# Kernel tuning notes

Hardware: AMD Instinct MI355X
Metric: run time of the kernel (lower is better)

## Reference

```python
import jax, jax.numpy as jnp
import numpy as np

B, T, D, H = 8, 2048, 1024, 1024

def setup_inputs() -> dict:
    key = jax.random.key(0)
    k1, k2, k3, k4 = jax.random.split(key, 4)
    scale = 1.0 / np.sqrt(D)
    return {
        "x": jax.random.normal(k1, (B, T, D), dtype=jnp.float32),
        "Wq": jax.random.normal(k2, (D, H), dtype=jnp.float32) * scale,
        "Wk": jax.random.normal(k3, (D, H), dtype=jnp.float32) * scale,
        "Wv": jax.random.normal(k4, (D, H), dtype=jnp.float32) * scale,
    }

def reference(x, Wq, Wk, Wv):
    # Single-head causal self-attention (dropout in eval mode = identity)
    q = jnp.einsum('btd,dh->bth', x, Wq)
    k = jnp.einsum('btd,dh->bth', x, Wk)
    v = jnp.einsum('btd,dh->bth', x, Wv)
    inv_sqrt_h = 1.0 / jnp.sqrt(jnp.asarray(q.shape[-1], q.dtype))
    scores = jnp.einsum('bqh,bkh->bqk', q, k) * inv_sqrt_h  # [B, T, T]
    Tq = scores.shape[-1]
    causal = jnp.tril(jnp.ones((Tq, Tq), dtype=bool))
    scores = jnp.where(causal, scores, jnp.asarray(-jnp.inf, scores.dtype))
    weights = jax.nn.softmax(scores, axis=-1)
    return jnp.einsum('bqk,bkh->bqh', weights, v)
```

## Files before the change

### kernel.cpp

```cpp
#include <hip/hip_runtime.h>

#define Bn 8
#define Tn 2048
#define Dn 1024
#define Hn 1024
#define Mn (Bn * Tn)

typedef __attribute__((ext_vector_type(8))) short bf16x8;
typedef __attribute__((ext_vector_type(4))) short short4v;
typedef __attribute__((ext_vector_type(16))) float f32x16;
typedef __attribute__((ext_vector_type(4))) float f32x4;

__device__ __forceinline__ unsigned short f2bf(float f) {
  union { float f; unsigned int u; } v; v.f = f;
  unsigned int u = v.u;
  u += 0x7FFFu + ((u >> 16) & 1u);
  return (unsigned short)(u >> 16);
}
__device__ __forceinline__ float bf2f(unsigned short h) {
  union { unsigned int u; float f; } v; v.u = ((unsigned int)h) << 16;
  return v.f;
}

__device__ __forceinline__ void gload_lds16(const unsigned short* g, unsigned short* l) {
  __builtin_amdgcn_global_load_lds((const __attribute__((address_space(1))) void*)g,
                                   (__attribute__((address_space(3))) void*)l, 16, 0, 0);
}


__device__ __forceinline__ void stage128x32s(const unsigned short* gbase, size_t row_stride,
                                             unsigned short* lds, int wave, int lane) {
#pragma unroll
  for (int c = 0; c < 2; ++c) {
    int rl = c * 16 + (lane >> 2);
    int pos = (lane & 3) ^ (rl & 3) ^ ((rl >> 2) & 3);
    const unsigned short* g = gbase + (size_t)(wave * 32 + rl) * row_stride + pos * 8;
    gload_lds16(g, lds + (wave * 32 + c * 16) * 32);
  }
}
__device__ __forceinline__ void stage128x64s(const unsigned short* gbase, size_t row_stride,
                                             unsigned short* lds0, unsigned short* lds1,
                                             int wave, int lane) {
  stage128x32s(gbase, row_stride, lds0, wave, lane);
  stage128x32s(gbase + 32, row_stride, lds1, wave, lane);
}

__device__ __forceinline__ void stage256x32s(const unsigned short* gbase, size_t row_stride,
                                             unsigned short* lds, int wave, int lane) {
#pragma unroll
  for (int c = 0; c < 2; ++c) {
    int rl = c * 16 + (lane >> 2);
    int pos = (lane & 3) ^ (rl & 3) ^ ((rl >> 2) & 3);
    const unsigned short* g = gbase + (size_t)(wave * 32 + rl) * row_stride + pos * 8;
    gload_lds16(g, lds + (wave * 32 + c * 16) * 32);
  }
}

__device__ __forceinline__ void mma_bk32(const unsigned short* lA, const unsigned short* lB,
                                         int wr, int wc, int l32, int half,
                                         f32x16 acc[2][2]) {
#pragma unroll
  for (int kk = 0; kk < 2; ++kk) {
    const int pos = (kk * 2 + half) ^ (l32 & 3) ^ ((l32 >> 2) & 3);
    bf16x8 af[2], bfr[2];
#pragma unroll
    for (int m = 0; m < 2; ++m)
      af[m] = *(const bf16x8*)&lA[(wr + m * 32 + l32) * 32 + pos * 8];
#pragma unroll
    for (int n = 0; n < 2; ++n)
      bfr[n] = *(const bf16x8*)&lB[(wc + n * 32 + l32) * 32 + pos * 8];
#pragma unroll
    for (int m = 0; m < 2; ++m)
#pragma unroll
      for (int n = 0; n < 2; ++n)
        acc[m][n] = __builtin_amdgcn_mfma_f32_32x32x16_bf16(af[m], bfr[n], acc[m][n], 0, 0, 0);
  }
}

__global__ __launch_bounds__(256) void k_convert(const float* __restrict__ in,
                                                 unsigned short* __restrict__ out, int n4) {
  int idx = blockIdx.x * 256 + threadIdx.x;
  if (idx >= n4) return;
  float4 v = ((const float4*)in)[idx];
  short4v o;
  o.x = (short)f2bf(v.x); o.y = (short)f2bf(v.y);
  o.z = (short)f2bf(v.z); o.w = (short)f2bf(v.w);
  *(short4v*)(out + (size_t)idx * 4) = o;
}

__global__ __launch_bounds__(256) void k_cvt_w_t(const float* __restrict__ W0,
                                                 const float* __restrict__ W1,
                                                 const float* __restrict__ W2,
                                                 unsigned short* __restrict__ Wt3) {
  const int n0 = blockIdx.x * 64, k0 = blockIdx.y * 64, w = blockIdx.z;
  const float* W = (w == 0) ? W0 : (w == 1) ? W1 : W2;
  unsigned short* Wt = Wt3 + (size_t)w * Hn * Dn;
  __shared__ unsigned short lT[64 * 65];
  const int tid = threadIdx.x;
#pragma unroll
  for (int p = 0; p < 2; ++p) {
    int o = tid + p * 256;
    int r = o >> 3, c = (o & 7) * 8;
    const float* src = W + (size_t)(k0 + r) * Hn + n0 + c;
    float4 v0 = *(const float4*)src;
    float4 v1 = *(const float4*)(src + 4);
    unsigned short* d = &lT[r * 65 + c];
    d[0] = f2bf(v0.x); d[1] = f2bf(v0.y); d[2] = f2bf(v0.z); d[3] = f2bf(v0.w);
    d[4] = f2bf(v1.x); d[5] = f2bf(v1.y); d[6] = f2bf(v1.z); d[7] = f2bf(v1.w);
  }
  __syncthreads();
#pragma unroll
  for (int p = 0; p < 2; ++p) {
    int o = tid + p * 256;
    int r2 = o >> 3, c2 = (o & 7) * 8;
    bf16x8 v;
#pragma unroll
    for (int s = 0; s < 8; ++s) v[s] = (short)lT[(c2 + s) * 65 + r2];
    *(bf16x8*)(Wt + (size_t)(n0 + r2) * Dn + k0 + c2) = v;
  }
}

__global__ __launch_bounds__(512, 2) void gemm_qkv(const unsigned short* __restrict__ A,
                                                   const unsigned short* __restrict__ Wt3,
                                                   unsigned short* __restrict__ Q,
                                                   unsigned short* __restrict__ Kb,
                                                   unsigned short* __restrict__ Vt) {
  const int f = blockIdx.x;
  const int c = f & 7;
  const int q = f >> 3;
  const int nn = q % 12;
  const int w = nn >> 2;
  const int n0 = (nn & 3) * 256;
  const int m0 = ((q / 12) * 8 + c) * 256;
  const unsigned short* Bw = Wt3 + (size_t)w * Hn * Dn;
  __shared__ unsigned short lds[2][4][256 * 32];
  const int tid = threadIdx.x;
  const int lane = tid & 63, wave = tid >> 6;
  const int wr = (wave >> 2) * 128;
  const int wc = (wave & 3) * 64;
  const int rl15 = lane & 15, l4 = lane >> 4;
  const int csw = (l4 ^ (lane & 3) ^ ((lane >> 2) & 3)) & 3;

  f32x4 acc[8][4];
#pragma unroll
  for (int m = 0; m < 8; ++m)
#pragma unroll
    for (int n = 0; n < 4; ++n) acc[m][n] = (f32x4)(0.f);

  const unsigned short* Ab = A + (size_t)m0 * Dn;
  const unsigned short* Bb = Bw + (size_t)n0 * Dn;

  auto stage_tile = [&](int kt, int d) {
#pragma unroll
    for (int h = 0; h < 2; ++h) {
      stage256x32s(Ab + kt * 64 + h * 32, Dn, &lds[d][h][0], wave, lane);
      stage256x32s(Bb + kt * 64 + h * 32, Dn, &lds[d][2 + h][0], wave, lane);
    }
  };

  auto compute_tile = [&](int d) {
    const unsigned short* pa = &lds[d][0][0];
    const unsigned short* pb = &lds[d][2][0];
    bf16x8 af[4][2], bf[4][2];
#pragma unroll
    for (int m = 0; m < 4; ++m)
#pragma unroll
      for (int h = 0; h < 2; ++h)
        af[m][h] = *(const bf16x8*)&pa[h * 8192 + (wr + m * 16 + rl15) * 32 + csw * 8];
#pragma unroll
    for (int n = 0; n < 2; ++n)
#pragma unroll
      for (int h = 0; h < 2; ++h)
        bf[n][h] = *(const bf16x8*)&pb[h * 8192 + (wc + n * 16 + rl15) * 32 + csw * 8];
    __builtin_amdgcn_s_setprio(1);
#pragma unroll
    for (int m = 0; m < 4; ++m)
#pragma unroll
      for (int n = 0; n < 2; ++n)
#pragma unroll
        for (int h = 0; h < 2; ++h)
          acc[m][n] = __builtin_amdgcn_mfma_f32_16x16x32_bf16(af[m][h], bf[n][h], acc[m][n], 0, 0, 0);
    __builtin_amdgcn_s_setprio(0);
#pragma unroll
    for (int n = 2; n < 4; ++n)
#pragma unroll
      for (int h = 0; h < 2; ++h)
        bf[n][h] = *(const bf16x8*)&pb[h * 8192 + (wc + n * 16 + rl15) * 32 + csw * 8];
    __builtin_amdgcn_s_setprio(1);
#pragma unroll
    for (int m = 0; m < 4; ++m)
#pragma unroll
      for (int n = 2; n < 4; ++n)
#pragma unroll
        for (int h = 0; h < 2; ++h)
          acc[m][n] = __builtin_amdgcn_mfma_f32_16x16x32_bf16(af[m][h], bf[n][h], acc[m][n], 0, 0, 0);
    __builtin_amdgcn_s_setprio(0);
#pragma unroll
    for (int m = 0; m < 4; ++m)
#pragma unroll
      for (int h = 0; h < 2; ++h)
        af[m][h] = *(const bf16x8*)&pa[h * 8192 + (wr + (m + 4) * 16 + rl15) * 32 + csw * 8];
    __builtin_amdgcn_s_setprio(1);
#pragma unroll
    for (int m = 0; m < 4; ++m)
#pragma unroll
      for (int n = 2; n < 4; ++n)
#pragma unroll
        for (int h = 0; h < 2; ++h)
          acc[m + 4][n] = __builtin_amdgcn_mfma_f32_16x16x32_bf16(af[m][h], bf[n][h], acc[m + 4][n], 0, 0, 0);
    __builtin_amdgcn_s_setprio(0);
    __builtin_amdgcn_s_setprio(1);
#pragma unroll
    for (int m = 0; m < 4; ++m)
#pragma unroll
      for (int n = 0; n < 2; ++n)
#pragma unroll
        for (int h = 0; h < 2; ++h)
          acc[m + 4][n] = __builtin_amdgcn_mfma_f32_16x16x32_bf16(af[m][h], bf[n][h], acc[m + 4][n], 0, 0, 0);
    __builtin_amdgcn_s_setprio(0);
  };

  stage_tile(0, 0);
  for (int kt = 0; kt < Dn / 64 - 1; ++kt) {
    const int d = kt & 1;
    __builtin_amdgcn_s_barrier();
    stage_tile(kt + 1, d ^ 1);
    asm volatile("s_waitcnt vmcnt(8)" ::: "memory");
    __builtin_amdgcn_s_barrier();
    compute_tile(d);
  }
  asm volatile("s_waitcnt vmcnt(0)" ::: "memory");
  __builtin_amdgcn_s_barrier();
  compute_tile(1);

  if (w != 2) {
    unsigned short* Cp = (w == 0) ? Q : Kb;
#pragma unroll
    for (int m = 0; m < 8; ++m) {
      const int row = m0 + wr + m * 16 + l4 * 4;
#pragma unroll
      for (int n = 0; n < 4; ++n) {
        const int col = n0 + wc + n * 16 + rl15;
#pragma unroll
        for (int r = 0; r < 4; ++r)
          Cp[(size_t)(row + r) * Hn + col] = f2bf(acc[m][n][r]);
      }
    }
  } else {
    const int bb = m0 >> 11;
    const int tb = m0 & 2047;
#pragma unroll
    for (int m = 0; m < 8; ++m) {
      const int t0 = tb + wr + m * 16 + l4 * 4;
#pragma unroll
      for (int n = 0; n < 4; ++n) {
        const int h = n0 + wc + n * 16 + rl15;
        short4v o;
        o.x = (short)f2bf(acc[m][n][0]);
        o.y = (short)f2bf(acc[m][n][1]);
        o.z = (short)f2bf(acc[m][n][2]);
        o.w = (short)f2bf(acc[m][n][3]);
        *(short4v*)(Vt + ((size_t)bb * Hn + h) * Tn + t0) = o;
      }
    }
  }
}

__global__ __launch_bounds__(256) void gemm_scores(const unsigned short* __restrict__ Q,
                                                   const unsigned short* __restrict__ K,
                                                   unsigned short* __restrict__ S) {
  const int f = blockIdx.x;
  const int b = f & 7;
  const int q = f >> 3;
  const int rt = 15 - (q & 15);
  const int ct = q >> 4;
  if (ct > rt) return;
  const int j0 = ct * 128, i0 = rt * 128;
  const unsigned short* Qb = Q + (size_t)b * Tn * Hn;
  const unsigned short* Kp = K + (size_t)b * Tn * Hn;
  unsigned short* Sb = S + (size_t)b * Tn * Tn;
  __shared__ unsigned short lA[2][128 * 32];
  __shared__ unsigned short lB[2][128 * 32];
  const int tid = threadIdx.x;
  const int lane = tid & 63, wave = tid >> 6;
  const int wr = (wave >> 1) * 64, wc = (wave & 1) * 64;
  const int l32 = lane & 31, half = lane >> 5;

  f32x16 acc[2][2];
#pragma unroll
  for (int m = 0; m < 2; ++m)
#pragma unroll
    for (int n = 0; n < 2; ++n) acc[m][n] = (f32x16)(0.f);

  for (int kt = 0; kt < Hn / 64; ++kt) {
    stage128x64s(Qb + (size_t)i0 * Hn + kt * 64, Hn, lA[0], lA[1], wave, lane);
    stage128x64s(Kp + (size_t)j0 * Hn + kt * 64, Hn, lB[0], lB[1], wave, lane);
    __syncthreads();
    mma_bk32(lA[0], lB[0], wr, wc, l32, half, acc);
    mma_bk32(lA[1], lB[1], wr, wc, l32, half, acc);
    __syncthreads();
  }
#pragma unroll
  for (int m = 0; m < 2; ++m)
#pragma unroll
    for (int n = 0; n < 2; ++n) {
      int col = j0 + wc + n * 32 + l32;
#pragma unroll
      for (int qd = 0; qd < 4; ++qd) {
        int rb = i0 + wr + m * 32 + 8 * qd + 4 * half;
#pragma unroll
        for (int rr = 0; rr < 4; ++rr) {
          int row = rb + rr;
          float e = (col <= row) ? __expf(acc[m][n][qd * 4 + rr] * 0.03125f) : 0.f;
          Sb[(size_t)row * Tn + col] = f2bf(e);
        }
      }
    }
}

__global__ __launch_bounds__(256) void k_rowsum(const unsigned short* __restrict__ S,
                                                float* __restrict__ l) {
  const int b = blockIdx.y;
  const int i = blockIdx.x * 4 + (threadIdx.x >> 6);
  const int lane = threadIdx.x & 63;
  const unsigned short* row = S + ((size_t)b * Tn + i) * (size_t)Tn;
  const int npad = ((i >> 7) + 1) << 7;
  float s = 0.f;
  for (int j0 = 0; j0 < npad; j0 += 512) {
    int j = j0 + lane * 8;
    if (j < npad) {
      bf16x8 v = *(const bf16x8*)(row + j);
#pragma unroll
      for (int t = 0; t < 8; ++t) s += bf2f((unsigned short)v[t]);
    }
  }
#pragma unroll
  for (int off = 32; off > 0; off >>= 1) s += __shfl_down(s, off);
  if (lane == 0) l[(size_t)b * Tn + i] = s;
}

__global__ __launch_bounds__(256) void gemm_out(const unsigned short* __restrict__ P,
                                                const unsigned short* __restrict__ Vt,
                                                const float* __restrict__ lbuf,
                                                float* __restrict__ O) {
  const int f = blockIdx.x;
  const int b = f & 7;
  const int q = f >> 3;
  const int n0 = (q & 7) * 128;
  const int rt = 15 - (q >> 3);
  const int i0 = rt * 128;
  const int nkt = (rt + 1) * 2;
  const unsigned short* Pb = P + (size_t)b * Tn * Tn;
  const unsigned short* Vb = Vt + (size_t)b * Tn * Hn;
  __shared__ unsigned short lA[2][128 * 32];
  __shared__ unsigned short lB[2][128 * 32];
  const int tid = threadIdx.x;
  const int lane = tid & 63, wave = tid >> 6;
  const int wr = (wave >> 1) * 64, wc = (wave & 1) * 64;
  const int l32 = lane & 31, half = lane >> 5;

  f32x16 acc[2][2];
#pragma unroll
  for (int m = 0; m < 2; ++m)
#pragma unroll
    for (int n = 0; n < 2; ++n) acc[m][n] = (f32x16)(0.f);

  for (int kt = 0; kt < nkt; ++kt) {
    stage128x64s(Pb + (size_t)i0 * Tn + kt * 64, Tn, lA[0], lA[1], wave, lane);
    stage128x64s(Vb + (size_t)n0 * Tn + kt * 64, Tn, lB[0], lB[1], wave, lane);
    __syncthreads();
    mma_bk32(lA[0], lB[0], wr, wc, l32, half, acc);
    mma_bk32(lA[1], lB[1], wr, wc, l32, half, acc);
    __syncthreads();
  }
#pragma unroll
  for (int m = 0; m < 2; ++m)
#pragma unroll
    for (int n = 0; n < 2; ++n) {
      int col = n0 + wc + n * 32 + l32;
#pragma unroll
      for (int qd = 0; qd < 4; ++qd) {
        int rb = i0 + wr + m * 32 + 8 * qd + 4 * half;
        float4 lv = *(const float4*)&lbuf[(size_t)b * Tn + rb];
#pragma unroll
        for (int rr = 0; rr < 4; ++rr) {
          float inv = 1.f / ((&lv.x)[rr]);
          O[((size_t)b * Tn + rb + rr) * Hn + col] = acc[m][n][qd * 4 + rr] * inv;
        }
      }
    }
}

extern "C" void kernel_launch(void* const* d_in, const int* in_sizes, int n_in,
                              void* d_out, int out_size, void* d_ws, size_t ws_size,
                              hipStream_t stream) {
  const float* x  = (const float*)d_in[0];
  const float* Wq = (const float*)d_in[1];
  const float* Wk = (const float*)d_in[2];
  const float* Wv = (const float*)d_in[3];
  float* out = (float*)d_out;

  char* ws = (char*)d_ws;
  const size_t MiB = 1024 * 1024;
  unsigned short* Wt3 = (unsigned short*)(ws + 0 * MiB);
  unsigned short* xb  = (unsigned short*)(ws + 6 * MiB);
  unsigned short* Qb  = (unsigned short*)(ws + 38 * MiB);
  unsigned short* Kb  = (unsigned short*)(ws + 70 * MiB);
  unsigned short* Vt  = (unsigned short*)(ws + 102 * MiB);
  unsigned short* S   = (unsigned short*)(ws + 134 * MiB);
  float*          lrow = (float*)(ws + 6 * MiB);

  {
    int n4 = (Mn * Dn) / 4;
    k_convert<<<dim3(n4 / 256), 256, 0, stream>>>(x, xb, n4);
  }
  {
    dim3 g(Hn / 64, Dn / 64, 3);
    k_cvt_w_t<<<g, 256, 0, stream>>>(Wq, Wk, Wv, Wt3);
  }
  {
    gemm_qkv<<<dim3(768), 512, 0, stream>>>(xb, Wt3, Qb, Kb, Vt);
  }
  {
    gemm_scores<<<dim3(2048), 256, 0, stream>>>(Qb, Kb, S);
  }
  {
    k_rowsum<<<dim3(Tn / 4, Bn), 256, 0, stream>>>(S, lrow);
  }
  {
    gemm_out<<<dim3(1024), 256, 0, stream>>>(S, Vt, lrow, out);
  }
}
```

Measured before the change: 349.2 us.

## Restructure QKV GEMM main loop into fine-grained interleaved stage/compute schedule

Replaces the double-buffered stage-then-compute loop of the QKV projection GEMM with a hand-scheduled pipeline. Each 32-wide half-tile load is interleaved with 16-MFMA compute chunks, with explicit barriers and lgkm/vm waitcnts, so loads into freed LDS sub-buffers overlap the compute. Register fragments also drop from 4x2 to 4 A plus 4 B. This aims to hide global-to-LDS latency better and lower register pressure, at the cost of many more barriers per K step and brittle manual waitcnt accounting.

```diff
diff --git a/kernel.cpp b/kernel.cpp
--- a/kernel.cpp
+++ b/kernel.cpp
@@ -76,6 +76,28 @@
         acc[m][n] = __builtin_amdgcn_mfma_f32_32x32x16_bf16(af[m], bfr[n], acc[m][n], 0, 0, 0);
   }
 }
+
+__device__ __forceinline__ void rd4(const unsigned short* p, int rbase, int rl15, int csw,
+                                    bf16x8 fr[4]) {
+#pragma unroll
+  for (int m = 0; m < 4; ++m)
+    fr[m] = *(const bf16x8*)&p[(rbase + m * 16 + rl15) * 32 + csw * 8];
+}
+
+__device__ __forceinline__ void mm16(const bf16x8 af[4], const bf16x8 bf[4], f32x4 ap[][4]) {
+  __builtin_amdgcn_s_setprio(1);
+#pragma unroll
+  for (int m = 0; m < 4; ++m)
+#pragma unroll
+    for (int n = 0; n < 4; ++n)
+      ap[m][n] = __builtin_amdgcn_mfma_f32_16x16x32_bf16(af[m], bf[n], ap[m][n], 0, 0, 0);
+  __builtin_amdgcn_s_setprio(0);
+}
+
+#define QKV_BAR  __builtin_amdgcn_s_barrier()
+#define QKV_LGKM asm volatile("s_waitcnt lgkmcnt(0)" ::: "memory")
+#define QKV_VM6  asm volatile("s_waitcnt vmcnt(6)" ::: "memory")
+#define QKV_VM0  asm volatile("s_waitcnt vmcnt(0)" ::: "memory")
 
 __global__ __launch_bounds__(256) void k_convert(const float* __restrict__ in,
                                                  unsigned short* __restrict__ out, int n4) {
@@ -150,88 +172,82 @@
   const unsigned short* Ab = A + (size_t)m0 * Dn;
   const unsigned short* Bb = Bw + (size_t)n0 * Dn;
 
-  auto stage_tile = [&](int kt, int d) {
-#pragma unroll
-    for (int h = 0; h < 2; ++h) {
-      stage256x32s(Ab + kt * 64 + h * 32, Dn, &lds[d][h][0], wave, lane);
-      stage256x32s(Bb + kt * 64 + h * 32, Dn, &lds[d][2 + h][0], wave, lane);
-    }
-  };
-
-  auto compute_tile = [&](int d) {
-    const unsigned short* pa = &lds[d][0][0];
-    const unsigned short* pb = &lds[d][2][0];
-    bf16x8 af[4][2], bf[4][2];
-#pragma unroll
-    for (int m = 0; m < 4; ++m)
-#pragma unroll
-      for (int h = 0; h < 2; ++h)
-        af[m][h] = *(const bf16x8*)&pa[h * 8192 + (wr + m * 16 + rl15) * 32 + csw * 8];
-#pragma unroll
-    for (int n = 0; n < 2; ++n)
-#pragma unroll
-      for (int h = 0; h < 2; ++h)
-        bf[n][h] = *(const bf16x8*)&pb[h * 8192 + (wc + n * 16 + rl15) * 32 + csw * 8];
-    __builtin_amdgcn_s_setprio(1);
-#pragma unroll
-    for (int m = 0; m < 4; ++m)
-#pragma unroll
-      for (int n = 0; n < 2; ++n)
-#pragma unroll
-        for (int h = 0; h < 2; ++h)
-          acc[m][n] = __builtin_amdgcn_mfma_f32_16x16x32_bf16(af[m][h], bf[n][h], acc[m][n], 0, 0, 0);
-    __builtin_amdgcn_s_setprio(0);
-#pragma unroll
-    for (int n = 2; n < 4; ++n)
-#pragma unroll
-      for (int h = 0; h < 2; ++h)
-        bf[n][h] = *(const bf16x8*)&pb[h * 8192 + (wc + n * 16 + rl15) * 32 + csw * 8];
-    __builtin_amdgcn_s_setprio(1);
-#pragma unroll
-    for (int m = 0; m < 4; ++m)
-#pragma unroll
-      for (int n = 2; n < 4; ++n)
-#pragma unroll
-        for (int h = 0; h < 2; ++h)
-          acc[m][n] = __builtin_amdgcn_mfma_f32_16x16x32_bf16(af[m][h], bf[n][h], acc[m][n], 0, 0, 0);
-    __builtin_amdgcn_s_setprio(0);
-#pragma unroll
-    for (int m = 0; m < 4; ++m)
-#pragma unroll
-      for (int h = 0; h < 2; ++h)
-        af[m][h] = *(const bf16x8*)&pa[h * 8192 + (wr + (m + 4) * 16 + rl15) * 32 + csw * 8];
-    __builtin_amdgcn_s_setprio(1);
-#pragma unroll
-    for (int m = 0; m < 4; ++m)
-#pragma unroll
-      for (int n = 2; n < 4; ++n)
-#pragma unroll
-        for (int h = 0; h < 2; ++h)
-          acc[m + 4][n] = __builtin_amdgcn_mfma_f32_16x16x32_bf16(af[m][h], bf[n][h], acc[m + 4][n], 0, 0, 0);
-    __builtin_amdgcn_s_setprio(0);
-    __builtin_amdgcn_s_setprio(1);
-#pragma unroll
-    for (int m = 0; m < 4; ++m)
-#pragma unroll
-      for (int n = 0; n < 2; ++n)
-#pragma unroll
-        for (int h = 0; h < 2; ++h)
-          acc[m + 4][n] = __builtin_amdgcn_mfma_f32_16x16x32_bf16(af[m][h], bf[n][h], acc[m + 4][n], 0, 0, 0);
-    __builtin_amdgcn_s_setprio(0);
-  };
-
-  stage_tile(0, 0);
-  for (int kt = 0; kt < Dn / 64 - 1; ++kt) {
-    const int d = kt & 1;
-    __builtin_amdgcn_s_barrier();
-    stage_tile(kt + 1, d ^ 1);
-    asm volatile("s_waitcnt vmcnt(8)" ::: "memory");
-    __builtin_amdgcn_s_barrier();
-    compute_tile(d);
-  }
-  asm volatile("s_waitcnt vmcnt(0)" ::: "memory");
-  __builtin_amdgcn_s_barrier();
-  compute_tile(1);
+  unsigned short* L0AL = &lds[0][0][0];
+  unsigned short* L0AH = &lds[0][1][0];
+  unsigned short* L0BL = &lds[0][2][0];
+  unsigned short* L0BH = &lds[0][3][0];
+  unsigned short* L1AL = &lds[1][0][0];
+  unsigned short* L1AH = &lds[1][1][0];
+  unsigned short* L1BL = &lds[1][2][0];
+  unsigned short* L1BH = &lds[1][3][0];
+
+  stage256x32s(Ab +  0, Dn, L0AL, wave, lane);
+  stage256x32s(Bb +  0, Dn, L0BL, wave, lane);
+  stage256x32s(Ab + 32, Dn, L0AH, wave, lane);
+  stage256x32s(Bb + 32, Dn, L0BH, wave, lane);
+  stage256x32s(Bb + 64, Dn, L1BL, wave, lane);
+  stage256x32s(Ab + 64, Dn, L1AL, wave, lane);
+  stage256x32s(Bb + 96, Dn, L1BH, wave, lane);
+  QKV_VM6;
+  QKV_BAR;
+
+  bf16x8 af[4], bf[4];
+#pragma unroll 1
+  for (int i = 0; i < 7; ++i) {
+    const int t1 = 2 * i + 1, t2 = 2 * i + 2, t3 = 2 * i + 3;
+    rd4(L0AL, wr, rl15, csw, af);
+    rd4(L0BL, wc, rl15, csw, bf);
+    stage256x32s(Ab + t1 * 64 + 32, Dn, L1AH, wave, lane);
+    QKV_BAR; QKV_LGKM; mm16(af, bf, &acc[0]); QKV_BAR;
+    rd4(L0AL, wr + 64, rl15, csw, af);
+    stage256x32s(Bb + t2 * 64, Dn, L0BL, wave, lane);
+    QKV_BAR; QKV_LGKM; mm16(af, bf, &acc[4]); QKV_BAR;
+    rd4(L0AH, wr, rl15, csw, af);
+    rd4(L0BH, wc, rl15, csw, bf);
+    stage256x32s(Ab + t2 * 64, Dn, L0AL, wave, lane);
+    QKV_BAR; QKV_LGKM; mm16(af, bf, &acc[0]); QKV_BAR;
+    rd4(L0AH, wr + 64, rl15, csw, af);
+    stage256x32s(Bb + t2 * 64 + 32, Dn, L0BH, wave, lane);
+    QKV_VM6;
+    QKV_BAR; QKV_LGKM; mm16(af, bf, &acc[4]); QKV_BAR;
+    rd4(L1AL, wr, rl15, csw, af);
+    rd4(L1BL, wc, rl15, csw, bf);
+    stage256x32s(Ab + t2 * 64 + 32, Dn, L0AH, wave, lane);
+    QKV_BAR; QKV_LGKM; mm16(af, bf, &acc[0]); QKV_BAR;
+    rd4(L1AL, wr + 64, rl15, csw, af);
+    stage256x32s(Bb + t3 * 64, Dn, L1BL, wave, lane);
+    QKV_BAR; QKV_LGKM; mm16(af, bf, &acc[4]); QKV_BAR;
+    rd4(L1AH, wr, rl15, csw, af);
+    rd4(L1BH, wc, rl15, csw, bf);
+    stage256x32s(Ab + t3 * 64, Dn, L1AL, wave, lane);
+    QKV_BAR; QKV_LGKM; mm16(af, bf, &acc[0]); QKV_BAR;
+    rd4(L1AH, wr + 64, rl15, csw, af);
+    stage256x32s(Bb + t3 * 64 + 32, Dn, L1BH, wave, lane);
+    QKV_VM6;
+    QKV_BAR; QKV_LGKM; mm16(af, bf, &acc[4]); QKV_BAR;
+  }
+  rd4(L0AL, wr, rl15, csw, af);
+  rd4(L0BL, wc, rl15, csw, bf);
+  stage256x32s(Ab + 15 * 64 + 32, Dn, L1AH, wave, lane);
+  QKV_BAR; QKV_LGKM; mm16(af, bf, &acc[0]); QKV_BAR;
+  rd4(L0AL, wr + 64, rl15, csw, af);
+  QKV_BAR; QKV_LGKM; mm16(af, bf, &acc[4]); QKV_BAR;
+  rd4(L0AH, wr, rl15, csw, af);
+  rd4(L0BH, wc, rl15, csw, bf);
+  QKV_BAR; QKV_LGKM; mm16(af, bf, &acc[0]); QKV_BAR;
+  rd4(L0AH, wr + 64, rl15, csw, af);
+  QKV_VM0;
+  QKV_BAR; QKV_LGKM; mm16(af, bf, &acc[4]); QKV_BAR;
+  rd4(L1AL, wr, rl15, csw, af);
+  rd4(L1BL, wc, rl15, csw, bf);
+  QKV_BAR; QKV_LGKM; mm16(af, bf, &acc[0]); QKV_BAR;
+  rd4(L1AL, wr + 64, rl15, csw, af);
+  QKV_BAR; QKV_LGKM; mm16(af, bf, &acc[4]); QKV_BAR;
+  rd4(L1AH, wr, rl15, csw, af);
+  rd4(L1BH, wc, rl15, csw, bf);
+  QKV_BAR; QKV_LGKM; mm16(af, bf, &acc[0]); QKV_BAR;
+  rd4(L1AH, wr + 64, rl15, csw, af);
+  QKV_LGKM; mm16(af, bf, &acc[4]);
 
   if (w != 2) {
     unsigned short* Cp = (w == 0) ? Q : Kb;
```

Result: faster. 334.2 us (-4.3%).
